# Performance work log

Hardware: AMD Instinct MI355X
Metric: run time of the kernel (lower is better)

Reference implementation:

```python
import jax, jax.numpy as jnp
import numpy as np

NEG_SLOPE = 0.2   # LeakyReLU default negative slope (GATv2 + nn.LeakyReLU)
K_NEIGH = 16      # att_args['num_neighs']


def leaky(x):
    return jnp.where(x >= 0, x, NEG_SLOPE * x)


def knn_idx(x_feat, y_feat, k):
    """Per-batch KNN of y in x (feature space). x_feat,y_feat: [B,M,C] -> [B,M,k] local idx into x."""
    d = (jnp.sum(y_feat * y_feat, -1, keepdims=True)
         - 2.0 * jnp.einsum('bmc,bnc->bmn', y_feat, x_feat)
         + jnp.sum(x_feat * x_feat, -1)[:, None, :])   # [B,M,M]
    _, idx = jax.lax.top_k(-d, k)
    return idx


def gatv2_bipartite(x_last, x_past, nbr, Wl, Wr, att_w):
    """Faithful GATv2Conv((last, past), edge_index) with flow='target_to_source',
    heads H, concat=False (mean over heads), bias=False, no self loops.
    x_j = lin_l(x[0]=last) gathered at knn neighbor (col) indices,
    x_i = lin_r(x[1]=past) at query (row) indices; each query has exactly K edges."""
    N, C = x_last.shape
    H = att_w.shape[0]
    xl = (x_last @ Wl).reshape(N, H, C)          # [N,H,C]
    xr = (x_past @ Wr).reshape(N, H, C)          # [N,H,C]
    xlj = xl[nbr]                                 # [N,K,H,C] gathered source msgs
    e = jnp.einsum('nkhc,hc->nkh', leaky(xlj + xr[:, None]), att_w)  # [N,K,H]
    a = jax.nn.softmax(e, axis=1)                 # softmax over each target's K edges
    out = jnp.einsum('nkh,nkhc->nhc', a, xlj)     # [N,H,C]
    return out.mean(axis=1)                       # concat=False -> head mean, [N,C]


def reference(pc_encoded_seq, W1, b1, W2, b2, Wl, Wr, att_w, batch_size, m_points):
    T, N, C = pc_encoded_seq.shape
    B, M = batch_size, m_points
    G = W2.shape[1]
    # node_level_proj (Linear-LeakyReLU-Linear-LeakyReLU) + global_mean_pool per frame
    h = leaky(leaky(pc_encoded_seq @ W1 + b1) @ W2 + b2)      # [T,N,G]
    global_fea = h.reshape(T, B, M, G).mean(axis=2)            # [T,B,G]
    # frame-level ScaledDotProductAttention: q = last frame, k=v = past frames
    q = global_fea[-1][:, None, :]                             # [B,1,G]
    kv = jnp.transpose(global_fea[:-1], (1, 0, 2))             # [B,T-1,G]
    score = jnp.einsum('bqg,btg->bqt', q, kv) / jnp.sqrt(jnp.asarray(G, jnp.float32))
    attn = jax.nn.softmax(score, axis=-1)                      # [B,1,T-1]
    last = pc_encoded_seq[-1]                                  # [N,C]
    lastb = last.reshape(B, M, C)
    offs = (jnp.arange(B) * M)[:, None, None]
    res = []
    for i in range(T - 1):   # small fixed frame count
        past = pc_encoded_seq[i]
        nbr = knn_idx(past.reshape(B, M, C), lastb, K_NEIGH) + offs  # global idx
        out = gatv2_bipartite(last, past, nbr.reshape(N, K_NEIGH), Wl, Wr, att_w)
        res.append(out.reshape(B, M, C))
    res = jnp.stack(res, axis=1)                               # [B,T-1,M,C]
    fw = attn[:, 0, :, None, None]                             # [B,T-1,1,1]
    weighted = jnp.sum(res * fw, axis=1)                       # [B,M,C]
    tm_out = jnp.concatenate([last, weighted.reshape(N, C)], axis=-1)  # [N,2C]
    return tm_out


def setup_inputs() -> dict:
    key = jax.random.key(0)
    ks = jax.random.split(key, 8)
    T, B, M, C, G, H = 5, 4, 4096, 128, 1024, 4
    N = B * M
    s = lambda fan: 1.0 / np.sqrt(fan)
    return {
        'pc_encoded_seq': jax.random.normal(ks[0], (T, N, C), jnp.float32),
        'W1': jax.random.normal(ks[1], (C, 128), jnp.float32) * s(C),
        'b1': jnp.zeros((128,), jnp.float32),
        'W2': jax.random.normal(ks[2], (128, G), jnp.float32) * s(128),
        'b2': jnp.zeros((G,), jnp.float32),
        'Wl': jax.random.normal(ks[3], (C, H * C), jnp.float32) * s(C),
        'Wr': jax.random.normal(ks[4], (C, H * C), jnp.float32) * s(C),
        'att_w': jax.random.normal(ks[5], (H, C), jnp.float32) * s(C),
        'batch_size': B,
        'm_points': M,
    }
```

## Files before the change

### kernel.cpp

```cpp
#include <hip/hip_runtime.h>
#include <hip/hip_bf16.h>
#include <hip/hip_fp16.h>


typedef __bf16 v8bf __attribute__((ext_vector_type(8)));
typedef float  v4f  __attribute__((ext_vector_type(4)));

__device__ __forceinline__ float lrelu(float x) { return fmaxf(x, 0.2f * x); }

__device__ __forceinline__ unsigned short f2bf(float x) {
  __hip_bfloat16 h = __float2bfloat16(x);
  return __builtin_bit_cast(unsigned short, h);
}
__device__ __forceinline__ float bf2f(unsigned short u) {
  unsigned int t = ((unsigned int)u) << 16;
  return __builtin_bit_cast(float, t);
}

#define GLOAD_LDS16(gp, lp)                                                   \
  __builtin_amdgcn_global_load_lds(                                           \
      (const __attribute__((address_space(1))) void*)(gp),                    \
      (__attribute__((address_space(3))) void*)(lp), 16, 0, 0)

template<int EP>
__global__ __launch_bounds__(256, 2)
void nt_mfma(const unsigned short* __restrict__ A, const unsigned short* __restrict__ B,
             const float* __restrict__ aux, void* __restrict__ outv, int K, int ldc)
{
  __shared__ __align__(16) unsigned short smem[8192];
  unsigned short* As = smem;
  unsigned short* Bs = smem + 4096;
  const int tid = threadIdx.x;
  const int l = tid & 63;
  const int w = tid >> 6;
  const int wm = w & 1, wn = w >> 1;
  const int m0 = blockIdx.y << 7, n0 = blockIdx.x << 7;
  const int fr = l & 15, quad = l >> 4;
  const int kt = K >> 5;

  const int r0 = tid >> 2, s0 = tid & 3;
  const unsigned short* Aa = A + (size_t)(m0 + r0) * K + s0 * 8;
  const unsigned short* Ab = A + (size_t)(m0 + r0 + 64) * K + s0 * 8;
  const unsigned short* Ba = B + (size_t)(n0 + r0) * K + s0 * 8;
  const unsigned short* Bb = B + (size_t)(n0 + r0 + 64) * K + s0 * 8;
  unsigned short* Ap0 = As + tid * 8;
  unsigned short* Ap1 = As + (tid + 256) * 8;
  unsigned short* Bp0 = Bs + tid * 8;
  unsigned short* Bp1 = Bs + (tid + 256) * 8;

  v4f acc[4][4];
#pragma unroll
  for (int i = 0; i < 4; ++i)
#pragma unroll
    for (int j = 0; j < 4; ++j) acc[i][j] = (v4f){0.f, 0.f, 0.f, 0.f};

  for (int ks = 0; ks < kt; ++ks) {
    GLOAD_LDS16(Aa + ks * 32, Ap0);
    GLOAD_LDS16(Ab + ks * 32, Ap1);
    GLOAD_LDS16(Ba + ks * 32, Bp0);
    GLOAD_LDS16(Bb + ks * 32, Bp1);
    __syncthreads();
    v8bf af[4], bf[4];
#pragma unroll
    for (int i = 0; i < 4; ++i)
      af[i] = *(const v8bf*)(As + (wm * 64 + i * 16 + fr) * 32 + quad * 8);
#pragma unroll
    for (int j = 0; j < 4; ++j)
      bf[j] = *(const v8bf*)(Bs + (wn * 64 + j * 16 + fr) * 32 + quad * 8);
#pragma unroll
    for (int i = 0; i < 4; ++i)
#pragma unroll
      for (int j = 0; j < 4; ++j)
        acc[i][j] = __builtin_amdgcn_mfma_f32_16x16x32_bf16(af[i], bf[j], acc[i][j], 0, 0, 0);
    __syncthreads();
  }

  if (EP == 1) {
    unsigned short* O = (unsigned short*)outv;
#pragma unroll
    for (int j = 0; j < 4; ++j) {
      int col = n0 + wn * 64 + j * 16 + fr;
      float bias = aux[col];
#pragma unroll
      for (int i = 0; i < 4; ++i) {
        int row = m0 + wm * 64 + i * 16 + quad * 4;
#pragma unroll
        for (int r = 0; r < 4; ++r)
          O[(size_t)(row + r) * ldc + col] = f2bf(lrelu(acc[i][j][r] + bias));
      }
    }
  } else if (EP == 2) {
    __syncthreads();
    float* red = (float*)smem;
#pragma unroll
    for (int j = 0; j < 4; ++j) {
      int lcol = wn * 64 + j * 16 + fr;
      float bias = aux[n0 + lcol];
      float s = 0.f;
#pragma unroll
      for (int i = 0; i < 4; ++i)
#pragma unroll
        for (int r = 0; r < 4; ++r) s += lrelu(acc[i][j][r] + bias);
      s += __shfl_xor(s, 16);
      s += __shfl_xor(s, 32);
      if (quad == 0) red[w * 128 + lcol] = s;
    }
    __syncthreads();
    if (tid < 128) {
      float s = (tid < 64) ? red[0 * 128 + tid] + red[1 * 128 + tid]
                           : red[2 * 128 + tid] + red[3 * 128 + tid];
      atomicAdd((float*)outv + ((m0 >> 12) << 10) + n0 + tid, s * (1.0f / 4096.0f));
    }
  } else {
    __half* O = (__half*)outv;
#pragma unroll
    for (int j = 0; j < 4; ++j) {
      int col = n0 + wn * 64 + j * 16 + fr;
#pragma unroll
      for (int i = 0; i < 4; ++i) {
        int row = m0 + wm * 64 + i * 16 + quad * 4;
#pragma unroll
        for (int r = 0; r < 4; ++r)
          O[(size_t)(row + r) * ldc + col] = __float2half(acc[i][j][r]);
      }
    }
  }
}

__global__ __launch_bounds__(256, 2)
void knn_fused(const unsigned short* __restrict__ ylay,
               const unsigned short* __restrict__ xlay,
               const float* __restrict__ xsq, int* __restrict__ nbrOut)
{
  __shared__ __align__(16) unsigned short As[4096];
  __shared__ __align__(16) unsigned short Bs[4096];
  __shared__ float candV[128 * 24];
  __shared__ int   candI[128 * 24];
  __shared__ float tauS[128];
  __shared__ int   cntS[128];
  __shared__ int   flagS;

  const int tid = threadIdx.x;
  const int l = tid & 63;
  const int w = tid >> 6;
  const int wm = w & 1, wn = w >> 1;
  const int pair = blockIdx.x >> 5;
  const int rb = blockIdx.x & 31;
  const int f = pair >> 2, b = pair & 3;
  const int m0 = rb << 7;
  const int fr = l & 15, quad = l >> 4;

  const unsigned short* A = ylay + (size_t)b * 4096 * 384;
  const unsigned short* B = xlay + ((size_t)f * 16384 + (size_t)b * 4096) * 384;
  const float* xq = xsq + f * 16384 + b * 4096;

  const int r0 = tid >> 2, s0 = tid & 3;
  const unsigned short* Aa = A + (size_t)(m0 + r0) * 384 + s0 * 8;
  const unsigned short* Ab = A + (size_t)(m0 + r0 + 64) * 384 + s0 * 8;
  unsigned short* Ap0 = As + tid * 8;
  unsigned short* Ap1 = As + (tid + 256) * 8;
  unsigned short* Bp0 = Bs + tid * 8;
  unsigned short* Bp1 = Bs + (tid + 256) * 8;

  float tv[16];
  int   ti[16];
#pragma unroll
  for (int k = 0; k < 16; ++k) { tv[k] = -3.0e38f; ti[k] = k; }
  float ownMin = -3.0e38f;
  int ownMinPos = 0;
  if (tid < 128) { tauS[tid] = -3.0e38f; cntS[tid] = 0; }
  if (tid == 0) flagS = 0;

  float tc[16];
#pragma unroll
  for (int i = 0; i < 16; ++i) tc[i] = -3.0e38f;
  __syncthreads();

  for (int ct = 0; ct < 32; ++ct) {
    const int n0 = ct << 7;
    const unsigned short* Ba = B + (size_t)(n0 + r0) * 384 + s0 * 8;
    const unsigned short* Bb = B + (size_t)(n0 + r0 + 64) * 384 + s0 * 8;

    v4f acc[4][4];
#pragma unroll
    for (int i = 0; i < 4; ++i)
#pragma unroll
      for (int j = 0; j < 4; ++j) acc[i][j] = (v4f){0.f, 0.f, 0.f, 0.f};

    for (int ks = 0; ks < 12; ++ks) {
      GLOAD_LDS16(Aa + ks * 32, Ap0);
      GLOAD_LDS16(Ab + ks * 32, Ap1);
      GLOAD_LDS16(Ba + ks * 32, Bp0);
      GLOAD_LDS16(Bb + ks * 32, Bp1);
      __syncthreads();
      v8bf af[4], bf[4];
#pragma unroll
      for (int i = 0; i < 4; ++i)
        af[i] = *(const v8bf*)(As + (wm * 64 + i * 16 + fr) * 32 + quad * 8);
#pragma unroll
      for (int j = 0; j < 4; ++j)
        bf[j] = *(const v8bf*)(Bs + (wn * 64 + j * 16 + fr) * 32 + quad * 8);
#pragma unroll
      for (int i = 0; i < 4; ++i)
#pragma unroll
        for (int j = 0; j < 4; ++j)
          acc[i][j] = __builtin_amdgcn_mfma_f32_16x16x32_bf16(af[i], bf[j], acc[i][j], 0, 0, 0);
      __syncthreads();
    }

    float xs[4];
#pragma unroll
    for (int j = 0; j < 4; ++j) xs[j] = xq[n0 + wn * 64 + j * 16 + fr];

    unsigned long long pushed = 0ull;
    for (;;) {
#pragma unroll
      for (int i = 0; i < 4; ++i)
#pragma unroll
        for (int r = 0; r < 4; ++r) {
          const int lrow = wm * 64 + i * 16 + quad * 4 + r;
          const float tau = tc[i * 4 + r];
#pragma unroll
          for (int j = 0; j < 4; ++j) {
            const int bit = i * 16 + j * 4 + r;
            float v = 2.f * acc[i][j][r] - xs[j];
            if (v > tau && !((pushed >> bit) & 1ull)) {
              int pos = atomicAdd(&cntS[lrow], 1);
              if (pos < 24) {
                candV[lrow * 24 + pos] = v;
                candI[lrow * 24 + pos] = n0 + wn * 64 + j * 16 + fr;
                pushed |= (1ull << bit);
              }
            }
          }
        }
      __syncthreads();
      if (tid < 128) {
        int c = cntS[tid];
        int cc = c < 24 ? c : 24;
        for (int q = 0; q < cc; ++q) {
          float v = candV[tid * 24 + q];
          if (v > ownMin) {
            tv[ownMinPos] = v;
            ti[ownMinPos] = candI[tid * 24 + q];
            ownMin = tv[0]; ownMinPos = 0;
#pragma unroll
            for (int k = 1; k < 16; ++k)
              if (tv[k] < ownMin) { ownMin = tv[k]; ownMinPos = k; }
          }
        }
        tauS[tid] = ownMin;
        if (c > 24) flagS = 1;
        cntS[tid] = 0;
      }
      __syncthreads();
#pragma unroll
      for (int i = 0; i < 4; ++i)
#pragma unroll
        for (int r = 0; r < 4; ++r)
          tc[i * 4 + r] = tauS[wm * 64 + i * 16 + quad * 4 + r];
      int ov = flagS;
      __syncthreads();
      if (tid == 0) flagS = 0;
      if (!ov) break;
    }
  }

  if (tid < 128) {
    const int base = b * 4096;
    int* outp = nbrOut + ((size_t)(f * 16384 + b * 4096) + m0 + tid) * 16;
#pragma unroll
    for (int k = 0; k < 16; ++k) outp[k] = base + ti[k];
  }
}

__global__ __launch_bounds__(256)
void convert_inputs(const float* __restrict__ seq, unsigned short* __restrict__ seqbf,
                    unsigned short* __restrict__ ylay, unsigned short* __restrict__ xlay,
                    float* __restrict__ xsq)
{
  const int tid = threadIdx.x;
  const int row = blockIdx.x * 8 + (tid >> 5);
  const int c4 = tid & 31;
  float4 v = *(const float4*)(seq + (size_t)row * 128 + c4 * 4);
  ushort4 hi, lo;
  hi.x = f2bf(v.x); lo.x = f2bf(v.x - bf2f(hi.x));
  hi.y = f2bf(v.y); lo.y = f2bf(v.y - bf2f(hi.y));
  hi.z = f2bf(v.z); lo.z = f2bf(v.z - bf2f(hi.z));
  hi.w = f2bf(v.w); lo.w = f2bf(v.w - bf2f(hi.w));
  *(ushort4*)(seqbf + (size_t)row * 128 + c4 * 4) = hi;
  float ss = v.x * v.x + v.y * v.y + v.z * v.z + v.w * v.w;
#pragma unroll
  for (int off = 16; off; off >>= 1) ss += __shfl_xor(ss, off);
  if (row < 65536) {
    unsigned short* p = xlay + (size_t)row * 384 + c4 * 4;
    *(ushort4*)(p) = hi; *(ushort4*)(p + 128) = lo; *(ushort4*)(p + 256) = hi;
    if (c4 == 0) xsq[row] = ss;
  } else {
    unsigned short* p = ylay + (size_t)(row - 65536) * 384 + c4 * 4;
    *(ushort4*)(p) = hi; *(ushort4*)(p + 128) = hi; *(ushort4*)(p + 256) = lo;
  }
}

__global__ __launch_bounds__(256)
void convert_weights(const float* __restrict__ W1, const float* __restrict__ W2,
                     const float* __restrict__ Wl, const float* __restrict__ Wr,
                     const float* __restrict__ aw,
                     unsigned short* __restrict__ W1t, unsigned short* __restrict__ W2t,
                     unsigned short* __restrict__ Wlv, unsigned short* __restrict__ Wrv,
                     __half* __restrict__ awh)
{
  int idx = blockIdx.x * 256 + threadIdx.x;
  if (idx < 16384) {
    int n = idx >> 7, k = idx & 127;
    W1t[idx] = f2bf(W1[k * 128 + n]);
  } else if (idx < 147456) {
    int i = idx - 16384; int n = i >> 7, k = i & 127;
    W2t[i] = f2bf(W2[k * 1024 + n]);
  } else if (idx < 344064) {
    int i = idx - 147456; int n = i / 384, k = i % 384;
    int s = k >> 7, kk = k & 127;
    float wv = Wl[kk * 512 + n];
    unsigned short h = f2bf(wv);
    Wlv[i] = (s == 1) ? f2bf(wv - bf2f(h)) : h;
  } else if (idx < 540672) {
    int i = idx - 344064; int n = i / 384, k = i % 384;
    int s = k >> 7, kk = k & 127;
    float wv = Wr[kk * 512 + n];
    unsigned short h = f2bf(wv);
    Wrv[i] = (s == 2) ? f2bf(wv - bf2f(h)) : h;
  } else if (idx < 541184) {
    int i = idx - 540672;
    awh[i] = __float2half(aw[i]);
  }
}

__global__ __launch_bounds__(1024)
void temporal_attn(const float* __restrict__ gfea, float* __restrict__ attnw)
{
  const int tid = threadIdx.x;
  const int w = tid >> 6, l = tid & 63;
  const int b = w >> 2, i = w & 3;
  const float* q  = gfea + (16 + b) * 1024;
  const float* kv = gfea + (i * 4 + b) * 1024;
  float p = 0.f;
  for (int g = l; g < 1024; g += 64) p += q[g] * kv[g];
#pragma unroll
  for (int off = 32; off; off >>= 1) p += __shfl_xor(p, off);
  __shared__ float sc[16];
  if (l == 0) sc[w] = p * 0.03125f;
  __syncthreads();
  if (tid < 4) {
    float v0 = sc[tid * 4 + 0], v1 = sc[tid * 4 + 1];
    float v2 = sc[tid * 4 + 2], v3 = sc[tid * 4 + 3];
    float mm = fmaxf(fmaxf(v0, v1), fmaxf(v2, v3));
    v0 = __expf(v0 - mm); v1 = __expf(v1 - mm);
    v2 = __expf(v2 - mm); v3 = __expf(v3 - mm);
    float inv = 1.f / (v0 + v1 + v2 + v3);
    attnw[tid * 4 + 0] = v0 * inv;
    attnw[tid * 4 + 1] = v1 * inv;
    attnw[tid * 4 + 2] = v2 * inv;
    attnw[tid * 4 + 3] = v3 * inv;
  }
}

__global__ __launch_bounds__(256)
void gat6(const __half* __restrict__ xlh, const __half* __restrict__ xrh,
          const int* __restrict__ nbr, const __half* __restrict__ awh,
          const float* __restrict__ attnw, float* __restrict__ wgt4)
{
  const int tid = threadIdx.x;
  const int l = tid & 63;
  const int blk = blockIdx.x;
  const int r8 = blk & 7;
  const int b = r8 >> 1;
  const int g = ((blk >> 3) << 1) | (r8 & 1);
  const int f = g >> 10;
  const int n4 = g & 1023;
  const int qid = f * 16384 + b * 4096 + n4 * 4 + (tid >> 6);
  const int h = l >> 4, cp = l & 15;
  const float fw = attnw[b * 4 + f] * 0.25f;

  const int jl = nbr[qid * 16 + (l & 15)];
  const __half* xbase = xlh + h * 128 + cp * 8;

  const __half2* xrp = (const __half2*)(xrh + (size_t)qid * 512 + h * 128 + cp * 8);
  float2 xr0 = __half22float2(xrp[0]), xr1 = __half22float2(xrp[1]);
  float2 xr2 = __half22float2(xrp[2]), xr3 = __half22float2(xrp[3]);
  const __half2* awp = (const __half2*)(awh + h * 128 + cp * 8);
  float2 aw0 = __half22float2(awp[0]), aw1 = __half22float2(awp[1]);
  float2 aw2 = __half22float2(awp[2]), aw3 = __half22float2(awp[3]);

  float m = -3.0e38f, s = 0.f;
  float o[8];
#pragma unroll
  for (int c = 0; c < 8; ++c) o[c] = 0.f;

  for (int ch = 0; ch < 2; ++ch) {
    float4 xv[8];
#pragma unroll
    for (int k = 0; k < 8; ++k) {
      int j = __shfl(jl, ch * 8 + k);
      xv[k] = *(const float4*)(xbase + (size_t)j * 512);
    }
    float e[8];
#pragma unroll
    for (int k = 0; k < 8; ++k) {
      const __half2* hp = (const __half2*)&xv[k];
      float2 x0 = __half22float2(hp[0]), x1 = __half22float2(hp[1]);
      float2 x2 = __half22float2(hp[2]), x3 = __half22float2(hp[3]);
      float p = 0.f;
      p += lrelu(x0.x + xr0.x) * aw0.x + lrelu(x0.y + xr0.y) * aw0.y;
      p += lrelu(x1.x + xr1.x) * aw1.x + lrelu(x1.y + xr1.y) * aw1.y;
      p += lrelu(x2.x + xr2.x) * aw2.x + lrelu(x2.y + xr2.y) * aw2.y;
      p += lrelu(x3.x + xr3.x) * aw3.x + lrelu(x3.y + xr3.y) * aw3.y;
      p += __shfl_xor(p, 1);
      p += __shfl_xor(p, 2);
      p += __shfl_xor(p, 4);
      p += __shfl_xor(p, 8);
      e[k] = p;
    }
    float mc = e[0];
#pragma unroll
    for (int k = 1; k < 8; ++k) mc = fmaxf(mc, e[k]);
    float mn = fmaxf(m, mc);
    float cr = __expf(m - mn);
    s *= cr;
#pragma unroll
    for (int c = 0; c < 8; ++c) o[c] *= cr;
#pragma unroll
    for (int k = 0; k < 8; ++k) {
      float a = __expf(e[k] - mn);
      s += a;
      const __half2* hp = (const __half2*)&xv[k];
      float2 f0 = __half22float2(hp[0]);
      float2 f1 = __half22float2(hp[1]);
      float2 f2 = __half22float2(hp[2]);
      float2 f3 = __half22float2(hp[3]);
      o[0] += a * f0.x; o[1] += a * f0.y;
      o[2] += a * f1.x; o[3] += a * f1.y;
      o[4] += a * f2.x; o[5] += a * f2.y;
      o[6] += a * f3.x; o[7] += a * f3.y;
    }
    m = mn;
  }

  const float sc = fw / s;
#pragma unroll
  for (int c = 0; c < 8; ++c) {
    float t = o[c] * sc;
    t += __shfl_xor(t, 16);
    t += __shfl_xor(t, 32);
    o[c] = t;
  }
  if (l < 16) {
    float* wp = wgt4 + (size_t)qid * 128 + l * 8;
    *(float4*)(wp)     = make_float4(o[0], o[1], o[2], o[3]);
    *(float4*)(wp + 4) = make_float4(o[4], o[5], o[6], o[7]);
  }
}

__global__ __launch_bounds__(256)
void finalize2(const float* __restrict__ last, const float* __restrict__ wgt4,
               float* __restrict__ out)
{
  int idx = blockIdx.x * 256 + threadIdx.x;
  int n = idx >> 6, q = idx & 63;
  float4 v;
  if (q < 32) {
    v = *(const float4*)(last + (size_t)n * 128 + 4 * q);
  } else {
    int c = (q - 32) * 4;
    v = make_float4(0.f, 0.f, 0.f, 0.f);
#pragma unroll
    for (int f = 0; f < 4; ++f) {
      float4 t = *(const float4*)(wgt4 + ((size_t)f * 16384 + n) * 128 + c);
      v.x += t.x; v.y += t.y; v.z += t.z; v.w += t.w;
    }
  }
  *(float4*)(out + (size_t)n * 256 + 4 * q) = v;
}

extern "C" void kernel_launch(void* const* d_in, const int* in_sizes, int n_in,
                              void* d_out, int out_size, void* d_ws, size_t ws_size,
                              hipStream_t stream)
{
  (void)in_sizes; (void)n_in; (void)out_size; (void)ws_size;
  const float* seq = (const float*)d_in[0];
  const float* W1  = (const float*)d_in[1];
  const float* b1  = (const float*)d_in[2];
  const float* W2  = (const float*)d_in[3];
  const float* b2  = (const float*)d_in[4];
  const float* Wl  = (const float*)d_in[5];
  const float* Wr  = (const float*)d_in[6];
  const float* aw  = (const float*)d_in[7];
  float* out = (float*)d_out;

  float* ws = (float*)d_ws;
  __half* xrh          = (__half*)ws;
  unsigned short* seqbf = (unsigned short*)(ws + 16777216);
  unsigned short* h1bf  = (unsigned short*)(ws + 22020096);
  __half* xlh           = (__half*)(ws + 22020096);
  unsigned short* ylay  = (unsigned short*)(ws + 27262976);
  unsigned short* xlay  = (unsigned short*)(ws + 30408704);
  float* wgt4           = ws + 30408704;
  float* gfea           = ws + 42991616;
  float* attn           = gfea + 20480;
  float* xsq            = attn + 16;
  int*   nbr            = (int*)(xsq + 65536);
  unsigned short* W1t   = (unsigned short*)(nbr + 1048576);
  unsigned short* W2t   = W1t + 16384;
  unsigned short* Wlv   = W2t + 131072;
  unsigned short* Wrv   = Wlv + 196608;
  __half* awh           = (__half*)(Wrv + 196608);

  (void)hipMemsetAsync(gfea, 0, 20480 * sizeof(float), stream);

  convert_inputs<<<10240, 256, 0, stream>>>(seq, seqbf, ylay, xlay, xsq);
  convert_weights<<<2114, 256, 0, stream>>>(W1, W2, Wl, Wr, aw, W1t, W2t, Wlv, Wrv, awh);

  nt_mfma<1><<<dim3(1, 640), 256, 0, stream>>>(seqbf, W1t, b1, h1bf, 128, 128);
  nt_mfma<2><<<dim3(8, 640), 256, 0, stream>>>(h1bf, W2t, b2, gfea, 128, 0);
  temporal_attn<<<1, 1024, 0, stream>>>(gfea, attn);

  knn_fused<<<512, 256, 0, stream>>>(ylay, xlay, xsq, nbr);

  nt_mfma<3><<<dim3(4, 128), 256, 0, stream>>>(ylay, Wlv, nullptr, xlh, 384, 512);
  nt_mfma<3><<<dim3(4, 512), 256, 0, stream>>>(xlay, Wrv, nullptr, xrh, 384, 512);

  gat6<<<16384, 256, 0, stream>>>(xlh, xrh, nbr, awh, attn, wgt4);

  finalize2<<<4096, 256, 0, stream>>>(seq + (size_t)4 * 16384 * 128, wgt4, out);
}
```

Baseline: 851.2 us.

## Triple-buffer LDS tiles with async prefetch and XOR swizzle in GEMM and KNN kernels

Both the generic bf16 MFMA GEMM and the fused KNN kernel now use a three-stage LDS ring. Global-to-LDS loads for tile k+2 are issued while tile k is computed, with explicit vmcnt waits and one barrier per k-step instead of two. The LDS column chunk is XOR-swizzled by row to cut bank conflicts on the fragment reads. In the KNN kernel the prefetch runs across column-tile boundaries, so the next tile loads during the top-k selection phase. The cost is three times the LDS per block, which may lower occupancy, and hand-written waitcnt synchronisation that is fragile.

```diff
diff --git a/kernel.cpp b/kernel.cpp
--- a/kernel.cpp
+++ b/kernel.cpp
@@ -22,14 +22,17 @@
       (const __attribute__((address_space(1))) void*)(gp),                    \
       (__attribute__((address_space(3))) void*)(lp), 16, 0, 0)
 
+#define RBAR() do { __builtin_amdgcn_s_barrier(); asm volatile("" ::: "memory"); } while (0)
+#define LBAR() do { asm volatile("s_waitcnt lgkmcnt(0)" ::: "memory");         \
+                    __builtin_amdgcn_s_barrier();                              \
+                    asm volatile("" ::: "memory"); } while (0)
+
 template<int EP>
 __global__ __launch_bounds__(256, 2)
 void nt_mfma(const unsigned short* __restrict__ A, const unsigned short* __restrict__ B,
              const float* __restrict__ aux, void* __restrict__ outv, int K, int ldc)
 {
-  __shared__ __align__(16) unsigned short smem[8192];
-  unsigned short* As = smem;
-  unsigned short* Bs = smem + 4096;
+  __shared__ __align__(16) unsigned short smem[3 * 8192];
   const int tid = threadIdx.x;
   const int l = tid & 63;
   const int w = tid >> 6;
@@ -37,16 +40,23 @@
   const int m0 = blockIdx.y << 7, n0 = blockIdx.x << 7;
   const int fr = l & 15, quad = l >> 4;
   const int kt = K >> 5;
-
-  const int r0 = tid >> 2, s0 = tid & 3;
-  const unsigned short* Aa = A + (size_t)(m0 + r0) * K + s0 * 8;
-  const unsigned short* Ab = A + (size_t)(m0 + r0 + 64) * K + s0 * 8;
-  const unsigned short* Ba = B + (size_t)(n0 + r0) * K + s0 * 8;
-  const unsigned short* Bb = B + (size_t)(n0 + r0 + 64) * K + s0 * 8;
-  unsigned short* Ap0 = As + tid * 8;
-  unsigned short* Ap1 = As + (tid + 256) * 8;
-  unsigned short* Bp0 = Bs + tid * 8;
-  unsigned short* Bp1 = Bs + (tid + 256) * 8;
+  const int xq4 = quad ^ ((fr >> 1) & 3);
+
+  const int r0 = tid >> 2;
+  const int sw = (tid & 3) ^ ((tid >> 3) & 3);
+  const unsigned short* Aa = A + (size_t)(m0 + r0) * K + sw * 8;
+  const unsigned short* Ab = Aa + (size_t)64 * K;
+  const unsigned short* Ba = B + (size_t)(n0 + r0) * K + sw * 8;
+  const unsigned short* Bb = Ba + (size_t)64 * K;
+
+  auto stage = [&](int bi, int ks) {
+    unsigned short* As = smem + bi * 8192;
+    unsigned short* Bs = As + 4096;
+    GLOAD_LDS16(Aa + ks * 32, As + tid * 8);
+    GLOAD_LDS16(Ab + ks * 32, As + (tid + 256) * 8);
+    GLOAD_LDS16(Ba + ks * 32, Bs + tid * 8);
+    GLOAD_LDS16(Bb + ks * 32, Bs + (tid + 256) * 8);
+  };
 
   v4f acc[4][4];
 #pragma unroll
@@ -54,25 +64,32 @@
 #pragma unroll
     for (int j = 0; j < 4; ++j) acc[i][j] = (v4f){0.f, 0.f, 0.f, 0.f};
 
+  stage(0, 0);
+  if (kt > 1) stage(1, 1);
+  int cur = 0, pend = (kt > 1) ? 2 : 1, sn = 2;
+
   for (int ks = 0; ks < kt; ++ks) {
-    GLOAD_LDS16(Aa + ks * 32, Ap0);
-    GLOAD_LDS16(Ab + ks * 32, Ap1);
-    GLOAD_LDS16(Ba + ks * 32, Bp0);
-    GLOAD_LDS16(Bb + ks * 32, Bp1);
-    __syncthreads();
-    v8bf af[4], bf[4];
+    if (pend == 2) asm volatile("s_waitcnt vmcnt(4)" ::: "memory");
+    else           asm volatile("s_waitcnt vmcnt(0)" ::: "memory");
+    RBAR();
+    int nb = cur + 2; if (nb >= 3) nb -= 3;
+    if (sn < kt) { stage(nb, sn); ++sn; } else { --pend; }
+    const unsigned short* As = smem + cur * 8192;
+    const unsigned short* Bs = As + 4096;
+    v8bf af[4], bfr[4];
 #pragma unroll
     for (int i = 0; i < 4; ++i)
-      af[i] = *(const v8bf*)(As + (wm * 64 + i * 16 + fr) * 32 + quad * 8);
+      af[i] = *(const v8bf*)(As + (wm * 64 + i * 16 + fr) * 32 + xq4 * 8);
 #pragma unroll
     for (int j = 0; j < 4; ++j)
-      bf[j] = *(const v8bf*)(Bs + (wn * 64 + j * 16 + fr) * 32 + quad * 8);
+      bfr[j] = *(const v8bf*)(Bs + (wn * 64 + j * 16 + fr) * 32 + xq4 * 8);
 #pragma unroll
     for (int i = 0; i < 4; ++i)
 #pragma unroll
       for (int j = 0; j < 4; ++j)
-        acc[i][j] = __builtin_amdgcn_mfma_f32_16x16x32_bf16(af[i], bf[j], acc[i][j], 0, 0, 0);
-    __syncthreads();
+        acc[i][j] = __builtin_amdgcn_mfma_f32_16x16x32_bf16(af[i], bfr[j], acc[i][j], 0, 0, 0);
+    __builtin_amdgcn_sched_barrier(0);
+    if (++cur == 3) cur = 0;
   }
 
   if (EP == 1) {
@@ -132,8 +149,7 @@
                const unsigned short* __restrict__ xlay,
                const float* __restrict__ xsq, int* __restrict__ nbrOut)
 {
-  __shared__ __align__(16) unsigned short As[4096];
-  __shared__ __align__(16) unsigned short Bs[4096];
+  __shared__ __align__(16) unsigned short smem[3 * 8192];
   __shared__ float candV[128 * 24];
   __shared__ int   candI[128 * 24];
   __shared__ float tauS[128];
@@ -149,18 +165,27 @@
   const int f = pair >> 2, b = pair & 3;
   const int m0 = rb << 7;
   const int fr = l & 15, quad = l >> 4;
+  const int xq4 = quad ^ ((fr >> 1) & 3);
 
   const unsigned short* A = ylay + (size_t)b * 4096 * 384;
   const unsigned short* B = xlay + ((size_t)f * 16384 + (size_t)b * 4096) * 384;
   const float* xq = xsq + f * 16384 + b * 4096;
 
-  const int r0 = tid >> 2, s0 = tid & 3;
-  const unsigned short* Aa = A + (size_t)(m0 + r0) * 384 + s0 * 8;
-  const unsigned short* Ab = A + (size_t)(m0 + r0 + 64) * 384 + s0 * 8;
-  unsigned short* Ap0 = As + tid * 8;
-  unsigned short* Ap1 = As + (tid + 256) * 8;
-  unsigned short* Bp0 = Bs + tid * 8;
-  unsigned short* Bp1 = Bs + (tid + 256) * 8;
+  const int r0 = tid >> 2;
+  const int sw = (tid & 3) ^ ((tid >> 3) & 3);
+  const unsigned short* Aa = A + (size_t)(m0 + r0) * 384 + sw * 8;
+  const unsigned short* Ab = Aa + 64 * 384;
+  const unsigned short* Brow = B + (size_t)r0 * 384 + sw * 8;
+
+  auto stage = [&](int bi, int ct, int ks) {
+    unsigned short* As = smem + bi * 8192;
+    unsigned short* Bs = As + 4096;
+    const unsigned short* Bt = Brow + ct * 49152 + ks * 32;
+    GLOAD_LDS16(Aa + ks * 32, As + tid * 8);
+    GLOAD_LDS16(Ab + ks * 32, As + (tid + 256) * 8);
+    GLOAD_LDS16(Bt, Bs + tid * 8);
+    GLOAD_LDS16(Bt + 64 * 384, Bs + (tid + 256) * 8);
+  };
 
   float tv[16];
   int   ti[16];
@@ -174,12 +199,18 @@
   float tc[16];
 #pragma unroll
   for (int i = 0; i < 16; ++i) tc[i] = -3.0e38f;
-  __syncthreads();
+
+  stage(0, 0, 0);
+  stage(1, 0, 1);
+  int cur = 0, pend = 2, sct = 0, sks = 2;
+
+  LBAR();
 
   for (int ct = 0; ct < 32; ++ct) {
     const int n0 = ct << 7;
-    const unsigned short* Ba = B + (size_t)(n0 + r0) * 384 + s0 * 8;
-    const unsigned short* Bb = B + (size_t)(n0 + r0 + 64) * 384 + s0 * 8;
+    float xs[4];
+#pragma unroll
+    for (int j = 0; j < 4; ++j) xs[j] = xq[n0 + wn * 64 + j * 16 + fr];
 
     v4f acc[4][4];
 #pragma unroll
@@ -188,29 +219,31 @@
       for (int j = 0; j < 4; ++j) acc[i][j] = (v4f){0.f, 0.f, 0.f, 0.f};
 
     for (int ks = 0; ks < 12; ++ks) {
-      GLOAD_LDS16(Aa + ks * 32, Ap0);
-      GLOAD_LDS16(Ab + ks * 32, Ap1);
-      GLOAD_LDS16(Ba + ks * 32, Bp0);
-      GLOAD_LDS16(Bb + ks * 32, Bp1);
-      __syncthreads();
-      v8bf af[4], bf[4];
+      if (pend == 2) asm volatile("s_waitcnt vmcnt(4)" ::: "memory");
+      else           asm volatile("s_waitcnt vmcnt(0)" ::: "memory");
+      RBAR();
+      int nb = cur + 2; if (nb >= 3) nb -= 3;
+      if (sct < 32) {
+        stage(nb, sct, sks);
+        if (++sks == 12) { sks = 0; ++sct; }
+      } else { --pend; }
+      const unsigned short* As = smem + cur * 8192;
+      const unsigned short* Bs = As + 4096;
+      v8bf af[4], bfr[4];
 #pragma unroll
       for (int i = 0; i < 4; ++i)
-        af[i] = *(const v8bf*)(As + (wm * 64 + i * 16 + fr) * 32 + quad * 8);
+        af[i] = *(const v8bf*)(As + (wm * 64 + i * 16 + fr) * 32 + xq4 * 8);
 #pragma unroll
       for (int j = 0; j < 4; ++j)
-        bf[j] = *(const v8bf*)(Bs + (wn * 64 + j * 16 + fr) * 32 + quad * 8);
+        bfr[j] = *(const v8bf*)(Bs + (wn * 64 + j * 16 + fr) * 32 + xq4 * 8);
 #pragma unroll
       for (int i = 0; i < 4; ++i)
 #pragma unroll
         for (int j = 0; j < 4; ++j)
-          acc[i][j] = __builtin_amdgcn_mfma_f32_16x16x32_bf16(af[i], bf[j], acc[i][j], 0, 0, 0);
-      __syncthreads();
-    }
-
-    float xs[4];
-#pragma unroll
-    for (int j = 0; j < 4; ++j) xs[j] = xq[n0 + wn * 64 + j * 16 + fr];
+          acc[i][j] = __builtin_amdgcn_mfma_f32_16x16x32_bf16(af[i], bfr[j], acc[i][j], 0, 0, 0);
+      __builtin_amdgcn_sched_barrier(0);
+      if (++cur == 3) cur = 0;
+    }
 
     unsigned long long pushed = 0ull;
     for (;;) {
@@ -234,7 +267,7 @@
             }
           }
         }
-      __syncthreads();
+      LBAR();
       if (tid < 128) {
         int c = cntS[tid];
         int cc = c < 24 ? c : 24;
@@ -253,14 +286,14 @@
         if (c > 24) flagS = 1;
         cntS[tid] = 0;
       }
-      __syncthreads();
+      LBAR();
 #pragma unroll
       for (int i = 0; i < 4; ++i)
 #pragma unroll
         for (int r = 0; r < 4; ++r)
           tc[i * 4 + r] = tauS[wm * 64 + i * 16 + quad * 4 + r];
       int ov = flagS;
-      __syncthreads();
+      LBAR();
       if (tid == 0) flagS = 0;
       if (!ov) break;
     }
```

New measurement: 857.3 us. No clear change (+0.7%).
